# Performance work log

Hardware: AMD Instinct MI355X
Metric: run time of the kernel (lower is better)

The kernel has to match this reference:

```python
import jax, jax.numpy as jnp
import numpy as np

CHUNK = 64


def _rmsnorm(x, g, eps=1e-6):
    return x * jax.lax.rsqrt(jnp.mean(x * x, axis=-1, keepdims=True) + eps) * g


def setup_inputs() -> dict:
    key = jax.random.key(0)
    ks = jax.random.split(key, 8)
    B, L, D, N = 4, 4096, 512, 64
    s = 0.02
    return {
        'x': jax.random.normal(ks[0], (B, L, D), jnp.float32),
        'A_log': -jnp.ones((D,), jnp.float32) * jnp.log(2.0),
        'dt_bias': jnp.log(jnp.expm1(jax.random.uniform(ks[1], (D,), jnp.float32, 0.001, 0.1))),
        'D_skip': jnp.ones((D,), jnp.float32),
        'W_xproj': jax.random.normal(ks[2], (D, 2 * D), jnp.float32) * s,
        'b_xproj': jnp.zeros((2 * D,), jnp.float32),
        'W_B': jax.random.normal(ks[3], (D, N), jnp.float32) * s,
        'W_C': jax.random.normal(ks[4], (D, N), jnp.float32) * s,
        'W_dt': jax.random.normal(ks[5], (D, D), jnp.float32) * s,
        'g_Bnorm': jnp.ones((N,), jnp.float32),
        'g_Cnorm': jnp.ones((N,), jnp.float32),
        'g_outnorm': jnp.ones((D,), jnp.float32),
        'W_out': jax.random.normal(ks[6], (D, D), jnp.float32) * s,
        'b_out': jnp.zeros((D,), jnp.float32),
    }


def reference(x, A_log, dt_bias, D_skip, W_xproj, b_xproj, W_B, W_C, W_dt,
              g_Bnorm, g_Cnorm, g_outnorm, W_out, b_out):
    b, l, d = x.shape
    n = W_B.shape[1]
    p = CHUNK
    c = l // p  # L chosen divisible by chunk size (original pads otherwise)

    A = -jnp.exp(jnp.clip(A_log, -20.0, 2.0))  # (d,)
    xp = x @ W_xproj + b_xproj                  # (b,l,2d)
    x_bar, z = jnp.split(xp, 2, axis=-1)
    Bm = _rmsnorm(x_bar @ W_B, g_Bnorm)         # (b,l,n)
    Cm = _rmsnorm(x_bar @ W_C, g_Cnorm)         # (b,l,n)
    dt = jnp.clip(jax.nn.softplus(x_bar @ W_dt + dt_bias), 1e-4, 5.0)
    A_bar = jnp.exp(jnp.clip(dt * A, -20.0, 0.0))  # (b,l,d)

    to_chunks = lambda t: t.reshape(b, c, p, t.shape[-1]).transpose(1, 0, 2, 3)
    xc, Bc, Cc, Ac = map(to_chunks, (x_bar, Bm, Cm, A_bar))  # (c,b,p,*)
    mask = jnp.tril(jnp.ones((p, p), x.dtype))

    def process_chunk(prev_state, inputs):
        x_c, B_c, C_c, A_c = inputs
        log_a = jnp.log(jnp.clip(A_c, 1e-8, 1.0))
        la_cs = jnp.cumsum(log_a, axis=1)  # (b,p,d)
        # intra-chunk decay matrix M: (b,p,p,d)
        M = jnp.exp(la_cs[:, :, None, :] - la_cs[:, None, :, :]) * mask[None, :, :, None]
        BX = jnp.einsum('bpn,bpd->bpnd', B_c, x_c)
        state = jnp.einsum('bijd,bjnd->bind', M, BX)
        y_intra = jnp.einsum('bpn,bpnd->bpd', C_c, state)
        decay = jnp.exp(la_cs)
        y_inter = jnp.einsum('bpn,bpnd->bpd', C_c,
                             prev_state[:, None, :, :] * decay[:, :, None, :])
        y_c = y_intra + y_inter
        a_total = jnp.exp(la_cs[:, -1, :])             # (b,d)
        a_to_end = jnp.exp(la_cs[:, -1:, :] - la_cs)   # (b,p,d)
        chunk_state = jnp.einsum('bpn,bpd->bnd', B_c, x_c * a_to_end)
        new_state = prev_state * a_total[:, None, :] + chunk_state
        new_state = jnp.where(jnp.isfinite(new_state), new_state, 0.0)
        y_c = jnp.where(jnp.isfinite(y_c), y_c, 0.0)
        return new_state, y_c

    init = jnp.zeros((b, n, d), x.dtype)
    _, yc = jax.lax.scan(jax.checkpoint(process_chunk), init, (xc, Bc, Cc, Ac))
    y = yc.transpose(1, 0, 2, 3).reshape(b, l, d)
    y = jnp.where(jnp.isfinite(y), y, 0.0)
    y = y + D_skip * x_bar
    y = _rmsnorm(y, g_outnorm) * jax.nn.silu(z)
    return y @ W_out + b_out
```

## Files before the change

kernel.cpp:

```cpp
#include <hip/hip_runtime.h>
#include <hip/hip_bf16.h>
#include <math.h>

typedef __hip_bfloat16 bf16;
typedef __attribute__((ext_vector_type(8))) short short8;
typedef __attribute__((ext_vector_type(4))) float floatx4;

#define B_ 4
#define L_ 4096
#define D_ 512
#define N_ 64
#define M_ (B_*L_)

__device__ __forceinline__ float b2f(bf16 v){ return __bfloat162float(v); }
__device__ __forceinline__ bf16  f2b(float v){ return __float2bfloat16(v); }
__device__ __forceinline__ short f2bs(float v){ bf16 h = __float2bfloat16(v); short s; __builtin_memcpy(&s,&h,2); return s; }

__global__ __launch_bounds__(1024) void k_transpose(const float* __restrict__ src,
                                                    bf16* __restrict__ dst, int K, int N){
    __shared__ float tile[32][33];
    int n0 = blockIdx.x*32, k0 = blockIdx.y*32;
    int tx = threadIdx.x, ty = threadIdx.y;
    tile[ty][tx] = src[(size_t)(k0+ty)*N + n0+tx];
    __syncthreads();
    ((short*)dst)[(size_t)(n0+ty)*K + k0+tx] = f2bs(tile[tx][ty]);
}

template<bool A_IS_F32>
__device__ __forceinline__ void gemm_tile_64x64(const void* __restrict__ Aptr,
                                                const bf16* __restrict__ Wt,
                                                int K, int m0, int n0,
                                                short (*As)[32], short (*Ns)[32],
                                                floatx4 acc[2][2]){
    int tid  = threadIdx.x;
    int w    = tid >> 6, lane = tid & 63;
    int wr   = w >> 1,  wc   = w & 1;
    int quad = lane >> 4, r16 = lane & 15;
    #pragma unroll
    for (int i=0;i<2;i++)
        #pragma unroll
        for (int j=0;j<2;j++)
            #pragma unroll
            for (int e=0;e<4;e++) acc[i][j][e] = 0.f;

    int lrow = tid >> 2, lkg = (tid & 3) * 8;
    for (int k0 = 0; k0 < K; k0 += 32){
        if (A_IS_F32){
            const float* ap = (const float*)Aptr + (size_t)(m0+lrow)*K + k0 + lkg;
            float4 a0 = *(const float4*)ap;
            float4 a1 = *(const float4*)(ap+4);
            short8 s;
            s[0]=f2bs(a0.x); s[1]=f2bs(a0.y); s[2]=f2bs(a0.z); s[3]=f2bs(a0.w);
            s[4]=f2bs(a1.x); s[5]=f2bs(a1.y); s[6]=f2bs(a1.z); s[7]=f2bs(a1.w);
            *(short8*)&As[lrow][lkg] = s;
        } else {
            *(short8*)&As[lrow][lkg] =
                *(const short8*)((const short*)Aptr + (size_t)(m0+lrow)*K + k0 + lkg);
        }
        *(short8*)&Ns[lrow][lkg] = *(const short8*)((const short*)Wt + (size_t)(n0+lrow)*K + k0 + lkg);
        __syncthreads();
        short8 af[2], bfr[2];
        #pragma unroll
        for (int t=0;t<2;t++) af[t]  = *(short8*)&As[wr*32 + t*16 + r16][quad*8];
        #pragma unroll
        for (int t=0;t<2;t++) bfr[t] = *(short8*)&Ns[wc*32 + t*16 + r16][quad*8];
        #pragma unroll
        for (int i=0;i<2;i++)
            #pragma unroll
            for (int j=0;j<2;j++)
                acc[i][j] = __builtin_amdgcn_mfma_f32_16x16x32_bf16(af[i], bfr[j], acc[i][j], 0,0,0);
        __syncthreads();
    }
}


__global__ __launch_bounds__(256) void k_xproj(const float* __restrict__ x,
        const bf16* __restrict__ Wt, const float* __restrict__ bias,
        float* __restrict__ xbar, bf16* __restrict__ siluz){
    __shared__ short As[64][32], Ns[64][32];
    floatx4 acc[2][2];
    int m0 = blockIdx.x*64, n0 = blockIdx.y*64;
    gemm_tile_64x64<true>(x, Wt, 512, m0, n0, As, Ns, acc);
    int tid=threadIdx.x, w=tid>>6, lane=tid&63, wr=w>>1, wc=w&1, quad=lane>>4, r16=lane&15;
    #pragma unroll
    for (int i=0;i<2;i++)
    #pragma unroll
    for (int j=0;j<2;j++)
    #pragma unroll
    for (int reg=0;reg<4;reg++){
        int gr = m0 + wr*32 + i*16 + quad*4 + reg;
        int gc = n0 + wc*32 + j*16 + r16;
        float v = acc[i][j][reg] + bias[gc];
        if (gc < 512){
            xbar[(size_t)gr*512 + gc] = v;
        } else {
            float s = v / (1.f + expf(-v));
            siluz[(size_t)gr*512 + (gc-512)] = f2b(s);
        }
    }
}

__global__ __launch_bounds__(256) void k_bcproj(const float* __restrict__ xbar,
        const bf16* __restrict__ WtB, const bf16* __restrict__ WtC,
        const float* __restrict__ gB, const float* __restrict__ gC,
        float* __restrict__ Bm, float* __restrict__ Cm){
    __shared__ short As[64][32], Ns[64][32];
    __shared__ float Ls[64][64];
    __shared__ float rfac[64];
    const bf16* Wt = blockIdx.y ? WtC : WtB;
    const float* g = blockIdx.y ? gC  : gB;
    float* outp    = blockIdx.y ? Cm  : Bm;
    floatx4 acc[2][2];
    int m0 = blockIdx.x*64;
    gemm_tile_64x64<true>(xbar, Wt, 512, m0, 0, As, Ns, acc);
    int tid=threadIdx.x, w=tid>>6, lane=tid&63, wr=w>>1, wc=w&1, quad=lane>>4, r16=lane&15;
    #pragma unroll
    for (int i=0;i<2;i++)
    #pragma unroll
    for (int j=0;j<2;j++)
    #pragma unroll
    for (int reg=0;reg<4;reg++)
        Ls[wr*32+i*16+quad*4+reg][wc*32+j*16+r16] = acc[i][j][reg];
    __syncthreads();
    if (tid < 64){
        float ss = 0.f;
        #pragma unroll
        for (int c=0;c<64;c++){ float t = Ls[tid][c]; ss += t*t; }
        rfac[tid] = rsqrtf(ss*(1.f/64.f) + 1e-6f);
    }
    __syncthreads();
    #pragma unroll
    for (int it=0; it<16; it++){
        int idx = it*256 + tid;
        int r = idx >> 6, cc = idx & 63;
        outp[(size_t)(m0+r)*64 + cc] = Ls[r][cc] * rfac[r] * g[cc];
    }
}

__global__ __launch_bounds__(256) void k_dtproj(const float* __restrict__ xbar,
        const bf16* __restrict__ Wt, const float* __restrict__ dt_bias,
        const float* __restrict__ A_log, float* __restrict__ la){
    __shared__ short As[64][32], Ns[64][32];
    floatx4 acc[2][2];
    int m0 = blockIdx.x*64, n0 = blockIdx.y*64;
    gemm_tile_64x64<true>(xbar, Wt, 512, m0, n0, As, Ns, acc);
    int tid=threadIdx.x, w=tid>>6, lane=tid&63, wr=w>>1, wc=w&1, quad=lane>>4, r16=lane&15;
    #pragma unroll
    for (int i=0;i<2;i++)
    #pragma unroll
    for (int j=0;j<2;j++)
    #pragma unroll
    for (int reg=0;reg<4;reg++){
        int gr = m0 + wr*32 + i*16 + quad*4 + reg;
        int gc = n0 + wc*32 + j*16 + r16;
        float v  = acc[i][j][reg] + dt_bias[gc];
        float sp = (v > 15.f) ? v : log1pf(expf(v));
        float dt = fminf(fmaxf(sp, 1e-4f), 5.f);
        float Ad = -expf(fminf(fmaxf(A_log[gc], -20.f), 2.f));
        float lav = fminf(fmaxf(dt*Ad, -18.420680743952367f), 0.f);
        la[(size_t)gr*512 + gc] = lav;
    }
}

__global__ __launch_bounds__(512) void k_chunkstate(const float* __restrict__ la,
        const float* __restrict__ xbar, const float* __restrict__ Bm,
        float* __restrict__ local, float* __restrict__ atot){
    int c = blockIdx.x, b = blockIdx.y, d = threadIdx.x;
    size_t rowbase = (size_t)b*L_ + (size_t)c*64;
    float cs[64];
    float s = 0.f;
    #pragma unroll
    for (int p=0;p<64;p++){ s += la[(rowbase+p)*512 + d]; cs[p] = s; }
    float cl = cs[63];
    size_t cb = (size_t)c*4 + b;
    atot[cb*512 + d] = expf(cl);
    #pragma unroll
    for (int p=0;p<64;p++)
        cs[p] = xbar[(rowbase+p)*512 + d] * expf(cl - cs[p]);
    const float* Bbase = Bm + rowbase*64;
    size_t obase = (cb*64)*512 + d;
    #pragma unroll 1
    for (int n4=0;n4<16;n4++){
        float a0=0.f,a1=0.f,a2=0.f,a3=0.f;
        #pragma unroll
        for (int p=0;p<64;p++){
            float4 bv = *(const float4*)(Bbase + (size_t)p*64 + n4*4);
            a0 += bv.x*cs[p]; a1 += bv.y*cs[p]; a2 += bv.z*cs[p]; a3 += bv.w*cs[p];
        }
        local[obase + (size_t)(n4*4+0)*512] = a0;
        local[obase + (size_t)(n4*4+1)*512] = a1;
        local[obase + (size_t)(n4*4+2)*512] = a2;
        local[obase + (size_t)(n4*4+3)*512] = a3;
    }
}

__global__ __launch_bounds__(256) void k_scan(float* __restrict__ local,
        const float* __restrict__ atot){
    int idx = blockIdx.x*256 + threadIdx.x;
    int d = idx & 511, n = (idx >> 9) & 63, b = idx >> 15;
    float s = 0.f;
    for (int c=0;c<64;c++){
        size_t cb = (size_t)c*4 + b;
        size_t off = (cb*64 + n)*512 + d;
        float v = local[off];
        local[off] = s;
        s = s * atot[cb*512 + d] + v;
        if (!isfinite(s)) s = 0.f;
    }
}

__global__ __launch_bounds__(512) void k_intra(const float* __restrict__ la,
        const float* __restrict__ xbar, const float* __restrict__ Bm,
        const float* __restrict__ Cm, const float* __restrict__ Sprev,
        float* __restrict__ y){
    int c = blockIdx.x, b = blockIdx.y, d = threadIdx.x;
    size_t cb = (size_t)c*4 + b;
    float st[64];
    #pragma unroll
    for (int n=0;n<64;n++) st[n] = Sprev[(cb*64 + n)*512 + d];
    size_t rowbase = (size_t)b*L_ + (size_t)c*64;
    #pragma unroll 1
    for (int i=0;i<64;i++){
        size_t row = rowbase + i;
        float ai = expf(la[row*512 + d]);
        float xi = xbar[row*512 + d];
        const float* Br = Bm + row*64;
        const float* Cr = Cm + row*64;
        float yv = 0.f;
        #pragma unroll
        for (int n4=0;n4<16;n4++){
            float4 bv = *(const float4*)(Br + n4*4);
            float4 cv = *(const float4*)(Cr + n4*4);
            st[n4*4+0] = ai*st[n4*4+0] + bv.x*xi;  yv += cv.x*st[n4*4+0];
            st[n4*4+1] = ai*st[n4*4+1] + bv.y*xi;  yv += cv.y*st[n4*4+1];
            st[n4*4+2] = ai*st[n4*4+2] + bv.z*xi;  yv += cv.z*st[n4*4+2];
            st[n4*4+3] = ai*st[n4*4+3] + bv.w*xi;  yv += cv.w*st[n4*4+3];
        }
        if (!isfinite(yv)) yv = 0.f;
        y[row*512 + d] = yv;
    }
}

__global__ __launch_bounds__(256) void k_outnorm(const float* __restrict__ y,
        const float* __restrict__ xbar, const float* __restrict__ Dskip,
        const float* __restrict__ g, const bf16* __restrict__ siluz,
        bf16* __restrict__ u){
    int wave = threadIdx.x >> 6, lane = threadIdx.x & 63;
    size_t row = (size_t)blockIdx.x*4 + wave;
    float v[8]; float ss = 0.f;
    #pragma unroll
    for (int j=0;j<8;j++){
        int d = j*64 + lane;
        float t = y[row*512 + d] + Dskip[d] * xbar[row*512 + d];
        v[j] = t; ss += t*t;
    }
    #pragma unroll
    for (int m=1;m<64;m<<=1) ss += __shfl_xor(ss, m, 64);
    float r = rsqrtf(ss*(1.f/512.f) + 1e-6f);
    #pragma unroll
    for (int j=0;j<8;j++){
        int d = j*64 + lane;
        u[row*512 + d] = f2b(v[j] * r * g[d] * b2f(siluz[row*512 + d]));
    }
}

__global__ __launch_bounds__(256) void k_outproj(const bf16* __restrict__ u,
        const bf16* __restrict__ Wt, const float* __restrict__ bias,
        float* __restrict__ out){
    __shared__ short As[64][32], Ns[64][32];
    floatx4 acc[2][2];
    int m0 = blockIdx.x*64, n0 = blockIdx.y*64;
    gemm_tile_64x64<false>(u, Wt, 512, m0, n0, As, Ns, acc);
    int tid=threadIdx.x, w=tid>>6, lane=tid&63, wr=w>>1, wc=w&1, quad=lane>>4, r16=lane&15;
    #pragma unroll
    for (int i=0;i<2;i++)
    #pragma unroll
    for (int j=0;j<2;j++)
    #pragma unroll
    for (int reg=0;reg<4;reg++){
        int gr = m0 + wr*32 + i*16 + quad*4 + reg;
        int gc = n0 + wc*32 + j*16 + r16;
        out[(size_t)gr*512 + gc] = acc[i][j][reg] + bias[gc];
    }
}

extern "C" void kernel_launch(void* const* d_in, const int* in_sizes, int n_in,
                              void* d_out, int out_size, void* d_ws, size_t ws_size,
                              hipStream_t stream){
    const float* x       = (const float*)d_in[0];
    const float* A_log   = (const float*)d_in[1];
    const float* dt_bias = (const float*)d_in[2];
    const float* D_skip  = (const float*)d_in[3];
    const float* W_xproj = (const float*)d_in[4];
    const float* b_xproj = (const float*)d_in[5];
    const float* W_B     = (const float*)d_in[6];
    const float* W_C     = (const float*)d_in[7];
    const float* W_dt    = (const float*)d_in[8];
    const float* g_B     = (const float*)d_in[9];
    const float* g_C     = (const float*)d_in[10];
    const float* g_out   = (const float*)d_in[11];
    const float* W_out   = (const float*)d_in[12];
    const float* b_out   = (const float*)d_in[13];
    float* out = (float*)d_out;

    char* wp = (char*)d_ws;
    auto alloc = [&](size_t bytes)->char*{ char* p = wp; wp += (bytes + 255) & ~(size_t)255; return p; };
    float* xbar  = (float*)alloc((size_t)M_*512*4);
    bf16*  siluz = (bf16*) alloc((size_t)M_*512*2);
    float* la    = (float*)alloc((size_t)M_*512*4);
    float* Bm    = (float*)alloc((size_t)M_*64*4);
    float* Cm    = (float*)alloc((size_t)M_*64*4);
    float* local = (float*)alloc((size_t)256*64*512*4);
    float* atot  = (float*)alloc((size_t)256*512*4);
    float* ybuf  = (float*)alloc((size_t)M_*512*4);
    bf16*  u     = (bf16*) alloc((size_t)M_*512*2);
    bf16*  WtX   = (bf16*) alloc((size_t)1024*512*2);
    bf16*  WtD   = (bf16*) alloc((size_t)512*512*2);
    bf16*  WtO   = (bf16*) alloc((size_t)512*512*2);
    bf16*  WtB   = (bf16*) alloc((size_t)64*512*2);
    bf16*  WtC   = (bf16*) alloc((size_t)64*512*2);

    dim3 tb(32,32);
    k_transpose<<<dim3(32,16), tb, 0, stream>>>(W_xproj, WtX, 512, 1024);
    k_transpose<<<dim3(16,16), tb, 0, stream>>>(W_dt,   WtD, 512, 512);
    k_transpose<<<dim3(16,16), tb, 0, stream>>>(W_out,  WtO, 512, 512);
    k_transpose<<<dim3(2,16),  tb, 0, stream>>>(W_B,    WtB, 512, 64);
    k_transpose<<<dim3(2,16),  tb, 0, stream>>>(W_C,    WtC, 512, 64);

    k_xproj     <<<dim3(M_/64, 16), 256, 0, stream>>>(x, WtX, b_xproj, xbar, siluz);
    k_bcproj    <<<dim3(M_/64, 2),  256, 0, stream>>>(xbar, WtB, WtC, g_B, g_C, Bm, Cm);
    k_dtproj    <<<dim3(M_/64, 8),  256, 0, stream>>>(xbar, WtD, dt_bias, A_log, la);
    k_chunkstate<<<dim3(64, 4),     512, 0, stream>>>(la, xbar, Bm, local, atot);
    k_scan      <<<512,             256, 0, stream>>>(local, atot);
    k_intra     <<<dim3(64, 4),     512, 0, stream>>>(la, xbar, Bm, Cm, local, ybuf);
    k_outnorm   <<<M_/4,            256, 0, stream>>>(ybuf, xbar, D_skip, g_out, siluz, u);
    k_outproj   <<<dim3(M_/64, 8),  256, 0, stream>>>(u, WtO, b_out, out);
}
```

Baseline: 399.3 us.

## Use 128x128 GEMM tiles, fuse chunk-state with intra scan, add MFMA inter-chunk pass

Replaces the three 64x64 GEMM kernels with one templated 128x128-tile GEMM that has padded shared memory. The xproj epilogue now also writes a bf16 copy of x_bar, so downstream GEMMs read half the bytes and skip the fp32-to-bf16 conversion. The chunk-state and intra-chunk kernels are merged into one pass that runs the recurrence from zero state: it emits the local intra-chunk output and the chunk-end state, and overwrites la with the cumulative decay. A new MFMA kernel then adds the inter-chunk contribution C·S_prev·decay, and the non-finite check moves into outnorm; running the inter-chunk term through bf16 MFMA adds rounding error.

```diff
diff --git a/kernel.cpp b/kernel.cpp
--- a/kernel.cpp
+++ b/kernel.cpp
@@ -9,12 +9,15 @@
 #define B_ 4
 #define L_ 4096
 #define D_ 512
-#define N_ 64
 #define M_ (B_*L_)
 
 __device__ __forceinline__ float b2f(bf16 v){ return __bfloat162float(v); }
 __device__ __forceinline__ bf16  f2b(float v){ return __float2bfloat16(v); }
 __device__ __forceinline__ short f2bs(float v){ bf16 h = __float2bfloat16(v); short s; __builtin_memcpy(&s,&h,2); return s; }
+__device__ __forceinline__ short8 cvt8(float4 a, float4 b){
+    short8 s; s[0]=f2bs(a.x); s[1]=f2bs(a.y); s[2]=f2bs(a.z); s[3]=f2bs(a.w);
+    s[4]=f2bs(b.x); s[5]=f2bs(b.y); s[6]=f2bs(b.z); s[7]=f2bs(b.w); return s;
+}
 
 __global__ __launch_bounds__(1024) void k_transpose(const float* __restrict__ src,
                                                     bf16* __restrict__ dst, int K, int N){
@@ -26,8 +29,82 @@
     ((short*)dst)[(size_t)(n0+ty)*K + k0+tx] = f2bs(tile[tx][ty]);
 }
 
-template<bool A_IS_F32>
-__device__ __forceinline__ void gemm_tile_64x64(const void* __restrict__ Aptr,
+template<int EPI, bool AF32>
+__global__ __launch_bounds__(256) void k_gemm128(const void* __restrict__ Ap,
+        const bf16* __restrict__ Wt, const float* __restrict__ bias,
+        const float* __restrict__ aux,
+        float* __restrict__ o1, bf16* __restrict__ o2, bf16* __restrict__ o3){
+    __shared__ short As[128][40];
+    __shared__ short Bs[128][40];
+    const int K = 512;
+    int m0 = blockIdx.x*128, n0 = blockIdx.y*128;
+    int tid=threadIdx.x, w=tid>>6, lane=tid&63;
+    int wr=w>>1, wc=w&1, quad=lane>>4, r16=lane&15;
+    floatx4 acc[4][4];
+    #pragma unroll
+    for (int i=0;i<4;i++)
+        #pragma unroll
+        for (int j=0;j<4;j++)
+            #pragma unroll
+            for (int e=0;e<4;e++) acc[i][j][e]=0.f;
+
+    int srow = tid>>1, scg = (tid&1)*16;
+    for (int k0=0;k0<K;k0+=32){
+        if (AF32){
+            const float* ap = (const float*)Ap + (size_t)(m0+srow)*K + k0 + scg;
+            float4 a0=*(const float4*)ap, a1=*(const float4*)(ap+4),
+                   a2=*(const float4*)(ap+8), a3=*(const float4*)(ap+12);
+            *(short8*)&As[srow][scg]   = cvt8(a0,a1);
+            *(short8*)&As[srow][scg+8] = cvt8(a2,a3);
+        } else {
+            const short* ap = (const short*)Ap + (size_t)(m0+srow)*K + k0 + scg;
+            *(short8*)&As[srow][scg]   = *(const short8*)ap;
+            *(short8*)&As[srow][scg+8] = *(const short8*)(ap+8);
+        }
+        const short* wp = (const short*)Wt + (size_t)(n0+srow)*K + k0 + scg;
+        *(short8*)&Bs[srow][scg]   = *(const short8*)wp;
+        *(short8*)&Bs[srow][scg+8] = *(const short8*)(wp+8);
+        __syncthreads();
+        short8 af[4], bv[4];
+        #pragma unroll
+        for (int i=0;i<4;i++) af[i] = *(short8*)&As[wr*64+i*16+r16][quad*8];
+        #pragma unroll
+        for (int j=0;j<4;j++) bv[j] = *(short8*)&Bs[wc*64+j*16+r16][quad*8];
+        #pragma unroll
+        for (int i=0;i<4;i++)
+            #pragma unroll
+            for (int j=0;j<4;j++)
+                acc[i][j] = __builtin_amdgcn_mfma_f32_16x16x32_bf16(af[i], bv[j], acc[i][j], 0,0,0);
+        __syncthreads();
+    }
+    #pragma unroll
+    for (int i=0;i<4;i++)
+    #pragma unroll
+    for (int j=0;j<4;j++)
+    #pragma unroll
+    for (int reg=0;reg<4;reg++){
+        int gr = m0 + wr*64 + i*16 + quad*4 + reg;
+        int gc = n0 + wc*64 + j*16 + r16;
+        float v = acc[i][j][reg] + bias[gc];
+        if (EPI==0){
+            if (gc < 512){
+                o1[(size_t)gr*512 + gc] = v;
+                o2[(size_t)gr*512 + gc] = f2b(v);
+            } else {
+                o3[(size_t)gr*512 + (gc-512)] = f2b(v / (1.f + expf(-v)));
+            }
+        } else if (EPI==1){
+            float sp = (v > 15.f) ? v : log1pf(expf(v));
+            float dt = fminf(fmaxf(sp, 1e-4f), 5.f);
+            float Ad = -expf(fminf(fmaxf(aux[gc], -20.f), 2.f));
+            o1[(size_t)gr*512 + gc] = fminf(fmaxf(dt*Ad, -18.420680743952367f), 0.f);
+        } else {
+            o1[(size_t)gr*512 + gc] = v;
+        }
+    }
+}
+
+__device__ __forceinline__ void gemm_tile_64x64(const bf16* __restrict__ Aptr,
                                                 const bf16* __restrict__ Wt,
                                                 int K, int m0, int n0,
                                                 short (*As)[32], short (*Ns)[32],
@@ -42,22 +119,10 @@
         for (int j=0;j<2;j++)
             #pragma unroll
             for (int e=0;e<4;e++) acc[i][j][e] = 0.f;
-
     int lrow = tid >> 2, lkg = (tid & 3) * 8;
     for (int k0 = 0; k0 < K; k0 += 32){
-        if (A_IS_F32){
-            const float* ap = (const float*)Aptr + (size_t)(m0+lrow)*K + k0 + lkg;
-            float4 a0 = *(const float4*)ap;
-            float4 a1 = *(const float4*)(ap+4);
-            short8 s;
-            s[0]=f2bs(a0.x); s[1]=f2bs(a0.y); s[2]=f2bs(a0.z); s[3]=f2bs(a0.w);
-            s[4]=f2bs(a1.x); s[5]=f2bs(a1.y); s[6]=f2bs(a1.z); s[7]=f2bs(a1.w);
-            *(short8*)&As[lrow][lkg] = s;
-        } else {
-            *(short8*)&As[lrow][lkg] =
-                *(const short8*)((const short*)Aptr + (size_t)(m0+lrow)*K + k0 + lkg);
-        }
-        *(short8*)&Ns[lrow][lkg] = *(const short8*)((const short*)Wt + (size_t)(n0+lrow)*K + k0 + lkg);
+        *(short8*)&As[lrow][lkg] = *(const short8*)((const short*)Aptr + (size_t)(m0+lrow)*K + k0 + lkg);
+        *(short8*)&Ns[lrow][lkg] = *(const short8*)((const short*)Wt   + (size_t)(n0+lrow)*K + k0 + lkg);
         __syncthreads();
         short8 af[2], bfr[2];
         #pragma unroll
@@ -73,34 +138,7 @@
     }
 }
 
-
-__global__ __launch_bounds__(256) void k_xproj(const float* __restrict__ x,
-        const bf16* __restrict__ Wt, const float* __restrict__ bias,
-        float* __restrict__ xbar, bf16* __restrict__ siluz){
-    __shared__ short As[64][32], Ns[64][32];
-    floatx4 acc[2][2];
-    int m0 = blockIdx.x*64, n0 = blockIdx.y*64;
-    gemm_tile_64x64<true>(x, Wt, 512, m0, n0, As, Ns, acc);
-    int tid=threadIdx.x, w=tid>>6, lane=tid&63, wr=w>>1, wc=w&1, quad=lane>>4, r16=lane&15;
-    #pragma unroll
-    for (int i=0;i<2;i++)
-    #pragma unroll
-    for (int j=0;j<2;j++)
-    #pragma unroll
-    for (int reg=0;reg<4;reg++){
-        int gr = m0 + wr*32 + i*16 + quad*4 + reg;
-        int gc = n0 + wc*32 + j*16 + r16;
-        float v = acc[i][j][reg] + bias[gc];
-        if (gc < 512){
-            xbar[(size_t)gr*512 + gc] = v;
-        } else {
-            float s = v / (1.f + expf(-v));
-            siluz[(size_t)gr*512 + (gc-512)] = f2b(s);
-        }
-    }
-}
-
-__global__ __launch_bounds__(256) void k_bcproj(const float* __restrict__ xbar,
+__global__ __launch_bounds__(256) void k_bcproj(const bf16* __restrict__ xbarh,
         const bf16* __restrict__ WtB, const bf16* __restrict__ WtC,
         const float* __restrict__ gB, const float* __restrict__ gC,
         float* __restrict__ Bm, float* __restrict__ Cm){
@@ -112,7 +150,7 @@
     float* outp    = blockIdx.y ? Cm  : Bm;
     floatx4 acc[2][2];
     int m0 = blockIdx.x*64;
-    gemm_tile_64x64<true>(xbar, Wt, 512, m0, 0, As, Ns, acc);
+    gemm_tile_64x64(xbarh, Wt, 512, m0, 0, As, Ns, acc);
     int tid=threadIdx.x, w=tid>>6, lane=tid&63, wr=w>>1, wc=w&1, quad=lane>>4, r16=lane&15;
     #pragma unroll
     for (int i=0;i<2;i++)
@@ -125,7 +163,7 @@
     if (tid < 64){
         float ss = 0.f;
         #pragma unroll
-        for (int c=0;c<64;c++){ float t = Ls[tid][c]; ss += t*t; }
+        for (int cc=0;cc<64;cc++){ float t = Ls[tid][cc]; ss += t*t; }
         rfac[tid] = rsqrtf(ss*(1.f/64.f) + 1e-6f);
     }
     __syncthreads();
@@ -137,61 +175,53 @@
     }
 }
 
-__global__ __launch_bounds__(256) void k_dtproj(const float* __restrict__ xbar,
-        const bf16* __restrict__ Wt, const float* __restrict__ dt_bias,
-        const float* __restrict__ A_log, float* __restrict__ la){
-    __shared__ short As[64][32], Ns[64][32];
-    floatx4 acc[2][2];
-    int m0 = blockIdx.x*64, n0 = blockIdx.y*64;
-    gemm_tile_64x64<true>(xbar, Wt, 512, m0, n0, As, Ns, acc);
-    int tid=threadIdx.x, w=tid>>6, lane=tid&63, wr=w>>1, wc=w&1, quad=lane>>4, r16=lane&15;
-    #pragma unroll
-    for (int i=0;i<2;i++)
-    #pragma unroll
-    for (int j=0;j<2;j++)
-    #pragma unroll
-    for (int reg=0;reg<4;reg++){
-        int gr = m0 + wr*32 + i*16 + quad*4 + reg;
-        int gc = n0 + wc*32 + j*16 + r16;
-        float v  = acc[i][j][reg] + dt_bias[gc];
-        float sp = (v > 15.f) ? v : log1pf(expf(v));
-        float dt = fminf(fmaxf(sp, 1e-4f), 5.f);
-        float Ad = -expf(fminf(fmaxf(A_log[gc], -20.f), 2.f));
-        float lav = fminf(fmaxf(dt*Ad, -18.420680743952367f), 0.f);
-        la[(size_t)gr*512 + gc] = lav;
-    }
-}
-
-__global__ __launch_bounds__(512) void k_chunkstate(const float* __restrict__ la,
+__global__ __launch_bounds__(512) void k_pass1(float* __restrict__ la_dec,
         const float* __restrict__ xbar, const float* __restrict__ Bm,
+        const float* __restrict__ Cm, float* __restrict__ ybuf,
         float* __restrict__ local, float* __restrict__ atot){
-    int c = blockIdx.x, b = blockIdx.y, d = threadIdx.x;
-    size_t rowbase = (size_t)b*L_ + (size_t)c*64;
-    float cs[64];
-    float s = 0.f;
-    #pragma unroll
-    for (int p=0;p<64;p++){ s += la[(rowbase+p)*512 + d]; cs[p] = s; }
-    float cl = cs[63];
-    size_t cb = (size_t)c*4 + b;
-    atot[cb*512 + d] = expf(cl);
-    #pragma unroll
-    for (int p=0;p<64;p++)
-        cs[p] = xbar[(rowbase+p)*512 + d] * expf(cl - cs[p]);
-    const float* Bbase = Bm + rowbase*64;
-    size_t obase = (cb*64)*512 + d;
-    #pragma unroll 1
-    for (int n4=0;n4<16;n4++){
-        float a0=0.f,a1=0.f,a2=0.f,a3=0.f;
-        #pragma unroll
-        for (int p=0;p<64;p++){
-            float4 bv = *(const float4*)(Bbase + (size_t)p*64 + n4*4);
-            a0 += bv.x*cs[p]; a1 += bv.y*cs[p]; a2 += bv.z*cs[p]; a3 += bv.w*cs[p];
+    int c=blockIdx.x, b=blockIdx.y, d=threadIdx.x;
+    size_t rowbase=(size_t)b*L_+(size_t)c*64;
+    size_t cb=(size_t)c*4+b;
+    float4 st[16];
+    #pragma unroll
+    for (int k=0;k<16;k++) st[k]=make_float4(0.f,0.f,0.f,0.f);
+    float cs=0.f, decv=0.f;
+    size_t off0 = rowbase*512 + d;
+    float la_n = la_dec[off0], x_n = xbar[off0];
+    #pragma unroll 2
+    for (int i=0;i<64;i++){
+        size_t off=(rowbase+i)*512+d;
+        float lai=la_n, xi=x_n;
+        if (i<63){ la_n=la_dec[off+512]; x_n=xbar[off+512]; }
+        float ai=__expf(lai);
+        cs += lai;
+        decv=__expf(cs);
+        la_dec[off]=decv;
+        const float* Br=Bm+(rowbase+i)*64;
+        const float* Cr=Cm+(rowbase+i)*64;
+        float4 yv=make_float4(0.f,0.f,0.f,0.f);
+        #pragma unroll
+        for (int k=0;k<16;k++){
+            float4 bv=*(const float4*)(Br+k*4);
+            float4 cv=*(const float4*)(Cr+k*4);
+            float4 s=st[k];
+            s.x=fmaf(ai,s.x,bv.x*xi); s.y=fmaf(ai,s.y,bv.y*xi);
+            s.z=fmaf(ai,s.z,bv.z*xi); s.w=fmaf(ai,s.w,bv.w*xi);
+            st[k]=s;
+            yv.x=fmaf(cv.x,s.x,yv.x); yv.y=fmaf(cv.y,s.y,yv.y);
+            yv.z=fmaf(cv.z,s.z,yv.z); yv.w=fmaf(cv.w,s.w,yv.w);
         }
-        local[obase + (size_t)(n4*4+0)*512] = a0;
-        local[obase + (size_t)(n4*4+1)*512] = a1;
-        local[obase + (size_t)(n4*4+2)*512] = a2;
-        local[obase + (size_t)(n4*4+3)*512] = a3;
-    }
+        ybuf[off]=(yv.x+yv.y)+(yv.z+yv.w);
+    }
+    #pragma unroll
+    for (int k=0;k<16;k++){
+        size_t ob=(cb*64 + k*4)*512 + d;
+        local[ob]        = st[k].x;
+        local[ob+512]    = st[k].y;
+        local[ob+1024]   = st[k].z;
+        local[ob+1536]   = st[k].w;
+    }
+    atot[cb*512+d]=decv;
 }
 
 __global__ __launch_bounds__(256) void k_scan(float* __restrict__ local,
@@ -209,35 +239,63 @@
     }
 }
 
-__global__ __launch_bounds__(512) void k_intra(const float* __restrict__ la,
-        const float* __restrict__ xbar, const float* __restrict__ Bm,
-        const float* __restrict__ Cm, const float* __restrict__ Sprev,
-        float* __restrict__ y){
-    int c = blockIdx.x, b = blockIdx.y, d = threadIdx.x;
-    size_t cb = (size_t)c*4 + b;
-    float st[64];
-    #pragma unroll
-    for (int n=0;n<64;n++) st[n] = Sprev[(cb*64 + n)*512 + d];
-    size_t rowbase = (size_t)b*L_ + (size_t)c*64;
-    #pragma unroll 1
-    for (int i=0;i<64;i++){
-        size_t row = rowbase + i;
-        float ai = expf(la[row*512 + d]);
-        float xi = xbar[row*512 + d];
-        const float* Br = Bm + row*64;
-        const float* Cr = Cm + row*64;
-        float yv = 0.f;
-        #pragma unroll
-        for (int n4=0;n4<16;n4++){
-            float4 bv = *(const float4*)(Br + n4*4);
-            float4 cv = *(const float4*)(Cr + n4*4);
-            st[n4*4+0] = ai*st[n4*4+0] + bv.x*xi;  yv += cv.x*st[n4*4+0];
-            st[n4*4+1] = ai*st[n4*4+1] + bv.y*xi;  yv += cv.y*st[n4*4+1];
-            st[n4*4+2] = ai*st[n4*4+2] + bv.z*xi;  yv += cv.z*st[n4*4+2];
-            st[n4*4+3] = ai*st[n4*4+3] + bv.w*xi;  yv += cv.w*st[n4*4+3];
-        }
-        if (!isfinite(yv)) yv = 0.f;
-        y[row*512 + d] = yv;
+__global__ __launch_bounds__(256) void k_inter(const float* __restrict__ Cm,
+        const float* __restrict__ Sprev, const float* __restrict__ dec,
+        float* __restrict__ ybuf){
+    __shared__ short Cs[64][72];
+    __shared__ short Ss[64][72];
+    int c=blockIdx.x, b=blockIdx.y, d0=blockIdx.z*64;
+    size_t rowbase=(size_t)b*L_+(size_t)c*64;
+    size_t cb=(size_t)c*4+b;
+    int tid=threadIdx.x, w=tid>>6, lane=tid&63;
+    int wr=w>>1, wc=w&1, quad=lane>>4, r16=lane&15;
+    {
+        int row=tid&63, cg=(tid>>6)*16;
+        const float* cp=Cm+(rowbase+row)*64+cg;
+        float4 c0=*(const float4*)cp, c1=*(const float4*)(cp+4),
+               c2=*(const float4*)(cp+8), c3=*(const float4*)(cp+12);
+        *(short8*)&Cs[row][cg]   = cvt8(c0,c1);
+        *(short8*)&Cs[row][cg+8] = cvt8(c2,c3);
+        int n=tid>>2, dg=(tid&3)*16;
+        const float* sp=Sprev+(cb*64+n)*512+d0+dg;
+        float4 v0=*(const float4*)sp, v1=*(const float4*)(sp+4),
+               v2=*(const float4*)(sp+8), v3=*(const float4*)(sp+12);
+        Ss[dg+ 0][n]=f2bs(v0.x); Ss[dg+ 1][n]=f2bs(v0.y); Ss[dg+ 2][n]=f2bs(v0.z); Ss[dg+ 3][n]=f2bs(v0.w);
+        Ss[dg+ 4][n]=f2bs(v1.x); Ss[dg+ 5][n]=f2bs(v1.y); Ss[dg+ 6][n]=f2bs(v1.z); Ss[dg+ 7][n]=f2bs(v1.w);
+        Ss[dg+ 8][n]=f2bs(v2.x); Ss[dg+ 9][n]=f2bs(v2.y); Ss[dg+10][n]=f2bs(v2.z); Ss[dg+11][n]=f2bs(v2.w);
+        Ss[dg+12][n]=f2bs(v3.x); Ss[dg+13][n]=f2bs(v3.y); Ss[dg+14][n]=f2bs(v3.z); Ss[dg+15][n]=f2bs(v3.w);
+    }
+    __syncthreads();
+    floatx4 acc[2][2];
+    #pragma unroll
+    for (int i=0;i<2;i++)
+        #pragma unroll
+        for (int j=0;j<2;j++)
+            #pragma unroll
+            for (int e=0;e<4;e++) acc[i][j][e]=0.f;
+    #pragma unroll
+    for (int ks=0;ks<2;ks++){
+        short8 af[2], bv[2];
+        #pragma unroll
+        for (int i=0;i<2;i++) af[i]=*(short8*)&Cs[wr*32+i*16+r16][ks*32+quad*8];
+        #pragma unroll
+        for (int j=0;j<2;j++) bv[j]=*(short8*)&Ss[wc*32+j*16+r16][ks*32+quad*8];
+        #pragma unroll
+        for (int i=0;i<2;i++)
+            #pragma unroll
+            for (int j=0;j<2;j++)
+                acc[i][j]=__builtin_amdgcn_mfma_f32_16x16x32_bf16(af[i],bv[j],acc[i][j],0,0,0);
+    }
+    #pragma unroll
+    for (int i=0;i<2;i++)
+    #pragma unroll
+    for (int j=0;j<2;j++)
+    #pragma unroll
+    for (int reg=0;reg<4;reg++){
+        int gi = wr*32+i*16+quad*4+reg;
+        int gd = d0+wc*32+j*16+r16;
+        size_t off=(rowbase+gi)*512+gd;
+        ybuf[off]=fmaf(dec[off],acc[i][j][reg],ybuf[off]);
     }
 }
 
@@ -251,7 +309,9 @@
     #pragma unroll
     for (int j=0;j<8;j++){
         int d = j*64 + lane;
-        float t = y[row*512 + d] + Dskip[d] * xbar[row*512 + d];
+        float yv = y[row*512 + d];
+        if (!isfinite(yv)) yv = 0.f;
+        float t = yv + Dskip[d] * xbar[row*512 + d];
         v[j] = t; ss += t*t;
     }
     #pragma unroll
@@ -261,26 +321,6 @@
     for (int j=0;j<8;j++){
         int d = j*64 + lane;
         u[row*512 + d] = f2b(v[j] * r * g[d] * b2f(siluz[row*512 + d]));
-    }
-}
-
-__global__ __launch_bounds__(256) void k_outproj(const bf16* __restrict__ u,
-        const bf16* __restrict__ Wt, const float* __restrict__ bias,
-        float* __restrict__ out){
-    __shared__ short As[64][32], Ns[64][32];
-    floatx4 acc[2][2];
-    int m0 = blockIdx.x*64, n0 = blockIdx.y*64;
-    gemm_tile_64x64<false>(u, Wt, 512, m0, n0, As, Ns, acc);
-    int tid=threadIdx.x, w=tid>>6, lane=tid&63, wr=w>>1, wc=w&1, quad=lane>>4, r16=lane&15;
-    #pragma unroll
-    for (int i=0;i<2;i++)
-    #pragma unroll
-    for (int j=0;j<2;j++)
-    #pragma unroll
-    for (int reg=0;reg<4;reg++){
-        int gr = m0 + wr*32 + i*16 + quad*4 + reg;
-        int gc = n0 + wc*32 + j*16 + r16;
-        out[(size_t)gr*512 + gc] = acc[i][j][reg] + bias[gc];
     }
 }
 
@@ -306,6 +346,7 @@
     char* wp = (char*)d_ws;
     auto alloc = [&](size_t bytes)->char*{ char* p = wp; wp += (bytes + 255) & ~(size_t)255; return p; };
     float* xbar  = (float*)alloc((size_t)M_*512*4);
+    bf16*  xbarh = (bf16*) alloc((size_t)M_*512*2);
     bf16*  siluz = (bf16*) alloc((size_t)M_*512*2);
     float* la    = (float*)alloc((size_t)M_*512*4);
     float* Bm    = (float*)alloc((size_t)M_*64*4);
@@ -327,12 +368,12 @@
     k_transpose<<<dim3(2,16),  tb, 0, stream>>>(W_B,    WtB, 512, 64);
     k_transpose<<<dim3(2,16),  tb, 0, stream>>>(W_C,    WtC, 512, 64);
 
-    k_xproj     <<<dim3(M_/64, 16), 256, 0, stream>>>(x, WtX, b_xproj, xbar, siluz);
-    k_bcproj    <<<dim3(M_/64, 2),  256, 0, stream>>>(xbar, WtB, WtC, g_B, g_C, Bm, Cm);
-    k_dtproj    <<<dim3(M_/64, 8),  256, 0, stream>>>(xbar, WtD, dt_bias, A_log, la);
-    k_chunkstate<<<dim3(64, 4),     512, 0, stream>>>(la, xbar, Bm, local, atot);
-    k_scan      <<<512,             256, 0, stream>>>(local, atot);
-    k_intra     <<<dim3(64, 4),     512, 0, stream>>>(la, xbar, Bm, Cm, local, ybuf);
-    k_outnorm   <<<M_/4,            256, 0, stream>>>(ybuf, xbar, D_skip, g_out, siluz, u);
-    k_outproj   <<<dim3(M_/64, 8),  256, 0, stream>>>(u, WtO, b_out, out);
-}
+    k_gemm128<0,true> <<<dim3(128, 8), 256, 0, stream>>>(x,     WtX, b_xproj, nullptr, xbar, xbarh, siluz);
+    k_bcproj          <<<dim3(256, 2), 256, 0, stream>>>(xbarh, WtB, WtC, g_B, g_C, Bm, Cm);
+    k_gemm128<1,false><<<dim3(128, 4), 256, 0, stream>>>(xbarh, WtD, dt_bias, A_log, la, nullptr, nullptr);
+    k_pass1           <<<dim3(64, 4),  512, 0, stream>>>(la, xbar, Bm, Cm, ybuf, local, atot);
+    k_scan            <<<512,          256, 0, stream>>>(local, atot);
+    k_inter           <<<dim3(64,4,8), 256, 0, stream>>>(Cm, local, la, ybuf);
+    k_outnorm         <<<M_/4,         256, 0, stream>>>(ybuf, xbar, D_skip, g_out, siluz, u);
+    k_gemm128<2,false><<<dim3(128, 4), 256, 0, stream>>>(u,     WtO, b_out, nullptr, out, nullptr, nullptr);
+}
```

Result: no change. 403.7 us (+1.1%).
